# Kernel optimization log

Hardware: AMD Instinct MI355X
Metric: run time of the kernel (lower is better)

## Reference

```python
import jax, jax.numpy as jnp
import numpy as np

DIM = 1024
HEADS = 16
HEAD_DIM = DIM // HEADS
B, N = 8, 1024


def setup_inputs() -> dict:
    key = jax.random.key(0)
    ks = jax.random.split(key, 10)
    s = lambda fan_in: 1.0 / np.sqrt(fan_in)
    return {
        "x": jax.random.normal(ks[0], (B, N, DIM), jnp.float32),
        "pose_angles": jax.random.normal(ks[1], (B, 3), jnp.float32),
        # weights stored (in, out) so y = x @ W + b (equivalent to torch Linear)
        "Wqkv": jax.random.normal(ks[2], (DIM, 3 * DIM), jnp.float32) * s(DIM),
        "bqkv": jnp.zeros((3 * DIM,), jnp.float32),
        "W1": jax.random.normal(ks[3], (3, 64), jnp.float32) * s(3),
        "b1": jnp.zeros((64,), jnp.float32),
        "W2": jax.random.normal(ks[4], (64, 3 * DIM), jnp.float32) * s(64),
        "b2": jnp.zeros((3 * DIM,), jnp.float32),
        "Wproj": jax.random.normal(ks[5], (DIM, DIM), jnp.float32) * s(DIM),
        "bproj": jnp.zeros((DIM,), jnp.float32),
    }


def reference(x, pose_angles, Wqkv, bqkv, W1, b1, W2, b2, Wproj, bproj):
    Bq, Nq, C = x.shape
    H, D = HEADS, HEAD_DIM
    # qkv projection -> [B,N,3,H,D] -> [3,B,H,N,D]
    qkv = (x @ Wqkv + bqkv).reshape(Bq, Nq, 3, H, D).transpose(2, 0, 3, 1, 4)
    q, k, v = qkv[0], qkv[1], qkv[2]
    # pose MLP: 3 -> 64 -> 3*dim, chunked into per-head biases [B,H,1,D]
    pose_emb = jax.nn.relu(pose_angles @ W1 + b1) @ W2 + b2
    pose_q, pose_k, pose_v = jnp.split(pose_emb, 3, axis=1)
    pose_q = pose_q.reshape(Bq, H, 1, D)
    pose_k = pose_k.reshape(Bq, H, 1, D)
    pose_v = pose_v.reshape(Bq, H, 1, D)
    q = q + pose_q
    k = k + pose_k
    v = v + pose_v
    scale = 1.0 / jnp.sqrt(jnp.asarray(D, x.dtype))
    attn = jax.nn.softmax(jnp.einsum("bhnd,bhmd->bhnm", q, k) * scale, axis=-1)
    # dropout is identity in eval mode
    out = jnp.einsum("bhnm,bhmd->bhnd", attn, v)
    out = out.transpose(0, 2, 1, 3).reshape(Bq, Nq, C)
    return out @ Wproj + bproj
```

## Files before the change

### kernel.cpp

```cpp
#include <hip/hip_runtime.h>
#include <stdint.h>

typedef unsigned short u16;
typedef short bf16x8 __attribute__((ext_vector_type(8)));
typedef short bf16x4 __attribute__((ext_vector_type(4)));
typedef float f32x4 __attribute__((ext_vector_type(4)));
typedef u16 u16x4 __attribute__((ext_vector_type(4)));

__device__ __forceinline__ u16 f2bf(float f) {
  union { float f; unsigned int u; } v; v.f = f;
  unsigned int r = v.u + 0x7fffu + ((v.u >> 16) & 1u);
  return (u16)(r >> 16);
}

__device__ __forceinline__ void async16(const void* g, void* l) {
  __builtin_amdgcn_global_load_lds(
      (const __attribute__((address_space(1))) unsigned int*)g,
      (__attribute__((address_space(3))) unsigned int*)l, 16, 0, 0);
}

__device__ __forceinline__ f32x4 mfma16x16(bf16x4 a, bf16x4 b, f32x4 c) {
#if __has_builtin(__builtin_amdgcn_mfma_f32_16x16x16bf16_1k)
  return __builtin_amdgcn_mfma_f32_16x16x16bf16_1k(a, b, c, 0, 0, 0);
#else
  asm volatile("v_mfma_f32_16x16x16_bf16 %0, %1, %2, %0\n\ts_nop 7\n\ts_nop 7"
               : "+v"(c) : "v"(a), "v"(b));
  return c;
#endif
}

__global__ void __launch_bounds__(256) front_kernel(
    const float4* __restrict__ x4, u16x4* __restrict__ xh4,
    const float* __restrict__ ang, const float* __restrict__ W1,
    const float* __restrict__ b1, const float* __restrict__ W2,
    const float* __restrict__ b2, float* __restrict__ pose,
    const float* __restrict__ Wqkv, u16* __restrict__ wqkvt,
    const float* __restrict__ Wproj, u16* __restrict__ wprojt) {
  __shared__ float sh[64 * 65];
  const int fb = blockIdx.x, t = threadIdx.x;
  if (fb < 96) {
    float (*hid)[64] = (float (*)[64])sh;
    for (int idx = t; idx < 512; idx += 256) {
      int b = idx >> 6, j = idx & 63;
      float a = b1[j];
#pragma unroll
      for (int i = 0; i < 3; ++i) a += ang[b * 3 + i] * W1[i * 64 + j];
      hid[b][j] = fmaxf(a, 0.f);
    }
    __syncthreads();
    int idx = fb * 256 + t;
    int b = idx / 3072, c = idx - b * 3072;
    float a = b2[c];
#pragma unroll
    for (int j = 0; j < 64; ++j) a += hid[b][j] * W2[j * 3072 + c];
    pose[idx] = a;
  } else if (fb < 1120) {
    const int n4 = 8 * 1024 * 1024 / 4;
    int i = (fb - 96) * 256 + t;
    const int stride = 1024 * 256;
    for (; i < n4; i += stride) {
      float4 v = x4[i];
      u16x4 o;
      o[0] = f2bf(v.x); o[1] = f2bf(v.y); o[2] = f2bf(v.z); o[3] = f2bf(v.w);
      xh4[i] = o;
    }
  } else {
    const float* W; u16* Wt; int Kdim, Ncol, bx, by;
    if (fb < 1888) { W = Wqkv; Wt = wqkvt; Kdim = 1024; Ncol = 3072;
                     int b = fb - 1120; bx = b % 48; by = b / 48; }
    else           { W = Wproj; Wt = wprojt; Kdim = 1024; Ncol = 1024;
                     int b = fb - 1888; bx = b % 16; by = b / 16; }
    float (*tile)[65] = (float (*)[65])sh;
    const int tx = t & 63, ty = t >> 6;
    const int c0 = bx * 64, k0 = by * 64;
#pragma unroll
    for (int rr = 0; rr < 16; ++rr) {
      int row = rr * 4 + ty;
      tile[row][tx] = W[(size_t)(k0 + row) * Ncol + c0 + tx];
    }
    __syncthreads();
#pragma unroll
    for (int rr = 0; rr < 16; ++rr) {
      int row = rr * 4 + ty;
      Wt[(size_t)(c0 + row) * Kdim + k0 + tx] = f2bf(tile[tx][row]);
    }
  }
}

__global__ void __launch_bounds__(512) gemm8_kernel(
    const u16* __restrict__ A, const u16* __restrict__ Bt,
    const float* __restrict__ bias, const float* __restrict__ pose,
    u16* __restrict__ qout, u16* __restrict__ kout, u16* __restrict__ vtout,
    int Kdim) {
  constexpr int BOFF = 256 * 64;
  __shared__ u16 lds[2][(256 + 128) * 64];
  const int t = threadIdx.x, l = t & 63, w = t >> 6;
  const int g = l >> 4, r16 = l & 15;
  const int wr = w >> 1, wc = w & 1;
  const int xk = r16 & 7;
  const int blk = blockIdx.x;
  const int xcd = blk & 7, c = blk >> 3;
  const int m0 = (xcd * 4 + (c & 3)) * 256;
  const int n0 = (c >> 2) * 128;
  const u16* Ab = A + (size_t)m0 * Kdim;
  const u16* Bb = Bt + (size_t)n0 * Kdim;

  auto stage = [&](int buf, int kt, int st) {
#pragma unroll
    for (int it = 0; it < 2; ++it) {
      int idx = it * 512 + t, row = idx >> 3;
      int seg = (idx & 7) ^ (row & 7);
      if (st < 2)
        async16(Ab + (size_t)(st * 128 + row) * Kdim + kt + seg * 8,
                &lds[buf][st * 128 * 64 + idx * 8]);
      else
        async16(Bb + (size_t)row * Kdim + kt + seg * 8, &lds[buf][BOFF + idx * 8]);
    }
  };

  f32x4 acc[4][4] = {};
  const int nT = Kdim >> 6;
#pragma unroll
  for (int st = 0; st < 3; ++st) stage(0, 0, st);

  for (int tt = 0; tt < nT; ++tt) {
    const int cur = tt & 1, nxt = cur ^ 1;
    const bool pf = (tt + 1 < nT);
    const int ktn = (tt + 1) << 6;
    if (pf) {
      stage(nxt, ktn, 0);
      __builtin_amdgcn_sched_barrier(0);
      asm volatile("s_waitcnt vmcnt(2)" ::: "memory");
    } else {
      asm volatile("s_waitcnt vmcnt(0)" ::: "memory");
    }
    __builtin_amdgcn_s_barrier();
    __builtin_amdgcn_sched_barrier(0);
    bf16x8 bfr[4][2], af[2][2];
#pragma unroll
    for (int nj = 0; nj < 4; ++nj)
#pragma unroll
      for (int ks = 0; ks < 2; ++ks)
        bfr[nj][ks] = *(const bf16x8*)&lds[cur][BOFF + (wc * 64 + nj * 16 + r16) * 64 +
                                               ((ks * 4 + g) ^ xk) * 8];
#pragma unroll
    for (int mi = 0; mi < 2; ++mi)
#pragma unroll
      for (int ks = 0; ks < 2; ++ks)
        af[mi][ks] = *(const bf16x8*)&lds[cur][(wr * 64 + mi * 16 + r16) * 64 +
                                              ((ks * 4 + g) ^ xk) * 8];
    __builtin_amdgcn_s_setprio(1);
#pragma unroll
    for (int ks = 0; ks < 2; ++ks)
#pragma unroll
      for (int mi = 0; mi < 2; ++mi)
#pragma unroll
        for (int nj = 0; nj < 4; ++nj)
          acc[mi][nj] = __builtin_amdgcn_mfma_f32_16x16x32_bf16(af[mi][ks], bfr[nj][ks],
                                                                acc[mi][nj], 0, 0, 0);
    __builtin_amdgcn_s_setprio(0);
    if (pf) { stage(nxt, ktn, 1); stage(nxt, ktn, 2); }
    bf16x8 af2[2][2];
#pragma unroll
    for (int mi = 0; mi < 2; ++mi)
#pragma unroll
      for (int ks = 0; ks < 2; ++ks)
        af2[mi][ks] = *(const bf16x8*)&lds[cur][(wr * 64 + (mi + 2) * 16 + r16) * 64 +
                                               ((ks * 4 + g) ^ xk) * 8];
    __builtin_amdgcn_s_setprio(1);
#pragma unroll
    for (int ks = 0; ks < 2; ++ks)
#pragma unroll
      for (int mi = 0; mi < 2; ++mi)
#pragma unroll
        for (int nj = 0; nj < 4; ++nj)
          acc[mi + 2][nj] = __builtin_amdgcn_mfma_f32_16x16x32_bf16(af2[mi][ks], bfr[nj][ks],
                                                                    acc[mi + 2][nj], 0, 0, 0);
    __builtin_amdgcn_s_setprio(0);
    __builtin_amdgcn_s_barrier();
  }

#pragma unroll
  for (int mi = 0; mi < 4; ++mi)
#pragma unroll
    for (int nj = 0; nj < 4; ++nj)
#pragma unroll
      for (int r = 0; r < 4; ++r) {
        int row = m0 + wr * 64 + mi * 16 + g * 4 + r;
        int col = n0 + wc * 64 + nj * 16 + r16;
        float v = acc[mi][nj][r] + bias[col];
        int b = row >> 10, n = row & 1023;
        v += pose[b * 3072 + col];
        u16 hv = f2bf(v);
        int three = col >> 10, hh = (col >> 6) & 15, d = col & 63;
        size_t bhh = (size_t)(b * 16 + hh);
        if (three == 0)      qout[(bhh * 1024 + n) * 64 + d] = hv;
        else if (three == 1) kout[(bhh * 1024 + n) * 64 + d] = hv;
        else                 vtout[(bhh * 64 + d) * 1024 + n] = hv;
      }
}

__global__ void __launch_bounds__(256) gemm97_kernel(
    const u16* __restrict__ A, const u16* __restrict__ Bt,
    const float* __restrict__ bias, float* __restrict__ cout,
    int Kdim, int Ncols) {
  __shared__ u16 ldsA[128 * 64];
  __shared__ u16 ldsB[128 * 64];
  const int t = threadIdx.x, l = t & 63, w = t >> 6;
  const int g = l >> 4, r16 = l & 15;
  const int wr = w >> 1, wc = w & 1;
  const int xk = r16 & 7;
  const int blk = blockIdx.x;
  const int xcd = blk & 7, c = blk >> 3;
  const int m0 = (xcd * 8 + (c & 7)) * 128;
  const int n0 = (c >> 3) * 128;
  const u16* Ab = A + (size_t)m0 * Kdim;
  const u16* Bb = Bt + (size_t)n0 * Kdim;

  f32x4 acc[4][4] = {};
  for (int kt = 0; kt < Kdim; kt += 64) {
#pragma unroll
    for (int ii = 0; ii < 4; ++ii) {
      int idx = ii * 256 + t, row = idx >> 3;
      int seg = (idx & 7) ^ (row & 7);
      async16(Ab + (size_t)row * Kdim + kt + seg * 8, &ldsA[idx * 8]);
    }
#pragma unroll
    for (int ii = 0; ii < 4; ++ii) {
      int idx = ii * 256 + t, row = idx >> 3;
      int seg = (idx & 7) ^ (row & 7);
      async16(Bb + (size_t)row * Kdim + kt + seg * 8, &ldsB[idx * 8]);
    }
    __syncthreads();
#pragma unroll
    for (int ks = 0; ks < 2; ++ks) {
      bf16x8 a[4], bb[4];
#pragma unroll
      for (int i = 0; i < 4; ++i)
        a[i] = *(const bf16x8*)&ldsA[(wr * 64 + i * 16 + r16) * 64 + ((ks * 4 + g) ^ xk) * 8];
#pragma unroll
      for (int j = 0; j < 4; ++j)
        bb[j] = *(const bf16x8*)&ldsB[(wc * 64 + j * 16 + r16) * 64 + ((ks * 4 + g) ^ xk) * 8];
#pragma unroll
      for (int i = 0; i < 4; ++i)
#pragma unroll
        for (int j = 0; j < 4; ++j)
          acc[i][j] = __builtin_amdgcn_mfma_f32_16x16x32_bf16(a[i], bb[j], acc[i][j], 0, 0, 0);
    }
    __syncthreads();
  }

#pragma unroll
  for (int i = 0; i < 4; ++i)
#pragma unroll
    for (int j = 0; j < 4; ++j)
#pragma unroll
      for (int r = 0; r < 4; ++r) {
        int row = m0 + wr * 64 + i * 16 + g * 4 + r;
        int col = n0 + wc * 64 + j * 16 + r16;
        cout[(size_t)row * Ncols + col] = acc[i][j][r] + bias[col];
      }
}

__global__ void __launch_bounds__(256) attn_kernel(
    const u16* __restrict__ Qb, const u16* __restrict__ Kb,
    const u16* __restrict__ Vtb, u16* __restrict__ aout) {
  __shared__ u16 ldsK[2][64][72];
  __shared__ u16 ldsV[2][64][72];
  const int t = threadIdx.x, l = t & 63, w = t >> 6;
  const int g = l >> 4, r16 = l & 15;
  const int blk = blockIdx.x;
  const int bh = blk & 127, qt = blk >> 7;
  const int b = bh >> 4, h = bh & 15;
  const int q0 = qt * 64 + w * 16;
  const u16* Qp = Qb + ((size_t)bh * 1024 + q0 + r16) * 64;
  bf16x8 qreg0 = *(const bf16x8*)(Qp + g * 8);
  bf16x8 qreg1 = *(const bf16x8*)(Qp + 32 + g * 8);
  const u16* Kbase = Kb + (size_t)bh * 1024 * 64;
  const u16* Vbase = Vtb + (size_t)bh * 64 * 1024;
  const float cexp = 0.18033688f;

  const int row0 = t >> 3, seg0 = t & 7;
  const int row1 = (256 + t) >> 3, seg1 = t & 7;
  bf16x8 kreg0, kreg1, vreg0, vreg1;
  auto gload = [&](int key0) {
    kreg0 = *(const bf16x8*)(Kbase + (size_t)(key0 + row0) * 64 + seg0 * 8);
    vreg0 = *(const bf16x8*)(Vbase + (size_t)row0 * 1024 + key0 + seg0 * 8);
    kreg1 = *(const bf16x8*)(Kbase + (size_t)(key0 + row1) * 64 + seg1 * 8);
    vreg1 = *(const bf16x8*)(Vbase + (size_t)row1 * 1024 + key0 + seg1 * 8);
  };
  auto lwrite = [&](int buf) {
    *(bf16x8*)&ldsK[buf][row0][seg0 * 8] = kreg0;
    *(bf16x8*)&ldsV[buf][row0][seg0 * 8] = vreg0;
    *(bf16x8*)&ldsK[buf][row1][seg1 * 8] = kreg1;
    *(bf16x8*)&ldsV[buf][row1][seg1 * 8] = vreg1;
  };

  float m = -3e38f, rs = 0.f;
  f32x4 o[4] = {};
  gload(0); lwrite(0);
  __syncthreads();
  int cur = 0;
  for (int kt = 0; kt < 16; ++kt) {
    const bool pf = (kt + 1 < 16);
    if (pf) gload((kt + 1) * 64);
    f32x4 s[4] = {};
#pragma unroll
    for (int f = 0; f < 4; ++f) {
      bf16x8 ak0 = *(const bf16x8*)&ldsK[cur][f * 16 + r16][g * 8];
      s[f] = __builtin_amdgcn_mfma_f32_16x16x32_bf16(ak0, qreg0, s[f], 0, 0, 0);
      bf16x8 ak1 = *(const bf16x8*)&ldsK[cur][f * 16 + r16][32 + g * 8];
      s[f] = __builtin_amdgcn_mfma_f32_16x16x32_bf16(ak1, qreg1, s[f], 0, 0, 0);
    }
    float mt = -3e38f;
#pragma unroll
    for (int f = 0; f < 4; ++f) {
      float m01 = fmaxf(s[f][0], s[f][1]);
      float m23 = fmaxf(s[f][2], s[f][3]);
      mt = fmaxf(mt, fmaxf(m01, m23));
    }
    mt = fmaxf(mt, __shfl_xor(mt, 16));
    mt = fmaxf(mt, __shfl_xor(mt, 32));
    if (!__all(mt - m <= 64.f)) {
      float mnew = fmaxf(m, mt);
      float alpha = exp2f((m - mnew) * cexp);
      float ar[4];
#pragma unroll
      for (int r = 0; r < 4; ++r) ar[r] = __shfl(alpha, (l & 48) | (g * 4 + r));
#pragma unroll
      for (int nf = 0; nf < 4; ++nf)
#pragma unroll
        for (int r = 0; r < 4; ++r) o[nf][r] *= ar[r];
      rs *= alpha;
      m = mnew;
    }
    const float nmc = -m * cexp;
    float rt = 0.f;
    bf16x4 pa[4];
#pragma unroll
    for (int f = 0; f < 4; ++f) {
#pragma unroll
      for (int r = 0; r < 4; ++r) {
        float p = exp2f(fmaf(s[f][r], cexp, nmc));
        rt += p;
        pa[f][r] = (short)f2bf(p);
      }
    }
    rt += __shfl_xor(rt, 16);
    rt += __shfl_xor(rt, 32);
    rs += rt;
#pragma unroll
    for (int s4 = 0; s4 < 4; ++s4)
#pragma unroll
      for (int nf = 0; nf < 4; ++nf) {
        bf16x4 bv = *(const bf16x4*)&ldsV[cur][nf * 16 + r16][s4 * 16 + g * 4];
        o[nf] = mfma16x16(pa[s4], bv, o[nf]);
      }
    if (pf) lwrite(cur ^ 1);
    __syncthreads();
    cur ^= 1;
  }
  float rr[4];
#pragma unroll
  for (int r = 0; r < 4; ++r) rr[r] = __shfl(1.0f / rs, (l & 48) | (g * 4 + r));
#pragma unroll
  for (int nf = 0; nf < 4; ++nf)
#pragma unroll
    for (int r = 0; r < 4; ++r) {
      int qq = qt * 64 + w * 16 + g * 4 + r;
      int d = nf * 16 + r16;
      aout[((size_t)b * 1024 + qq) * 1024 + h * 64 + d] = f2bf(o[nf][r] * rr[r]);
    }
}

extern "C" void kernel_launch(void* const* d_in, const int* in_sizes, int n_in,
                              void* d_out, int out_size, void* d_ws, size_t ws_size,
                              hipStream_t stream) {
  (void)in_sizes; (void)n_in; (void)out_size; (void)ws_size;
  const float* x     = (const float*)d_in[0];
  const float* ang   = (const float*)d_in[1];
  const float* Wqkv  = (const float*)d_in[2];
  const float* bqkv  = (const float*)d_in[3];
  const float* W1    = (const float*)d_in[4];
  const float* b1    = (const float*)d_in[5];
  const float* W2    = (const float*)d_in[6];
  const float* b2    = (const float*)d_in[7];
  const float* Wproj = (const float*)d_in[8];
  const float* bproj = (const float*)d_in[9];
  float* out = (float*)d_out;
  char* ws = (char*)d_ws;

  u16* xh     = (u16*)(ws);
  u16* wqkvt  = (u16*)(ws + (size_t)16 * 1024 * 1024);
  u16* wprojt = (u16*)(ws + (size_t)22 * 1024 * 1024);
  float* pose = (float*)(ws + (size_t)24 * 1024 * 1024);
  u16* Qb     = (u16*)(ws + (size_t)25 * 1024 * 1024);
  u16* Kb     = (u16*)(ws + (size_t)41 * 1024 * 1024);
  u16* Vtb    = (u16*)(ws + (size_t)57 * 1024 * 1024);

  front_kernel<<<2144, 256, 0, stream>>>((const float4*)x, (u16x4*)xh,
                                         ang, W1, b1, W2, b2, pose,
                                         Wqkv, wqkvt, Wproj, wprojt);
  gemm8_kernel<<<768, 512, 0, stream>>>(xh, wqkvt, bqkv, pose,
                                        Qb, Kb, Vtb, 1024);
  attn_kernel<<<2048, 256, 0, stream>>>(Qb, Kb, Vtb, xh);
  gemm97_kernel<<<512, 256, 0, stream>>>(xh, wprojt, bproj, out, 1024, 1024);
}
```

Before: 200.5 us.

## Process two query tiles per wave to reuse K/V LDS tiles

Each wave now handles 32 query rows as two 16-row halves that share the same K/V tiles staged in LDS, which doubles the block's query tile to 128 and halves the grid to 1024 blocks. This halves global K/V traffic and LDS staging per query, and also moves the row-sum cross-lane reduction out of the loop to a single pass at the end. The cost is more registers for two accumulator sets, possibly lower occupancy, and fewer blocks to spread across CUs.

```diff
diff --git a/kernel.cpp b/kernel.cpp
--- a/kernel.cpp
+++ b/kernel.cpp
@@ -272,10 +272,13 @@
   const int blk = blockIdx.x;
   const int bh = blk & 127, qt = blk >> 7;
   const int b = bh >> 4, h = bh & 15;
-  const int q0 = qt * 64 + w * 16;
-  const u16* Qp = Qb + ((size_t)bh * 1024 + q0 + r16) * 64;
-  bf16x8 qreg0 = *(const bf16x8*)(Qp + g * 8);
-  bf16x8 qreg1 = *(const bf16x8*)(Qp + 32 + g * 8);
+  const int q0 = qt * 128 + w * 32;
+  const u16* QpA = Qb + ((size_t)bh * 1024 + q0 + r16) * 64;
+  const u16* QpB = Qb + ((size_t)bh * 1024 + q0 + 16 + r16) * 64;
+  bf16x8 qA0 = *(const bf16x8*)(QpA + g * 8);
+  bf16x8 qA1 = *(const bf16x8*)(QpA + 32 + g * 8);
+  bf16x8 qB0 = *(const bf16x8*)(QpB + g * 8);
+  bf16x8 qB1 = *(const bf16x8*)(QpB + 32 + g * 8);
   const u16* Kbase = Kb + (size_t)bh * 1024 * 64;
   const u16* Vbase = Vtb + (size_t)bh * 64 * 1024;
   const float cexp = 0.18033688f;
@@ -296,21 +299,18 @@
     *(bf16x8*)&ldsV[buf][row1][seg1 * 8] = vreg1;
   };
 
-  float m = -3e38f, rs = 0.f;
-  f32x4 o[4] = {};
-  gload(0); lwrite(0);
-  __syncthreads();
+  float mA = -3e38f, mB = -3e38f, rsA = 0.f, rsB = 0.f;
+  f32x4 oA[4] = {}, oB[4] = {};
   int cur = 0;
-  for (int kt = 0; kt < 16; ++kt) {
-    const bool pf = (kt + 1 < 16);
-    if (pf) gload((kt + 1) * 64);
+
+  auto half = [&](bf16x8 q0r, bf16x8 q1r, float& m, float& rs, f32x4 (&o)[4]) {
     f32x4 s[4] = {};
 #pragma unroll
     for (int f = 0; f < 4; ++f) {
       bf16x8 ak0 = *(const bf16x8*)&ldsK[cur][f * 16 + r16][g * 8];
-      s[f] = __builtin_amdgcn_mfma_f32_16x16x32_bf16(ak0, qreg0, s[f], 0, 0, 0);
+      s[f] = __builtin_amdgcn_mfma_f32_16x16x32_bf16(ak0, q0r, s[f], 0, 0, 0);
       bf16x8 ak1 = *(const bf16x8*)&ldsK[cur][f * 16 + r16][32 + g * 8];
-      s[f] = __builtin_amdgcn_mfma_f32_16x16x32_bf16(ak1, qreg1, s[f], 0, 0, 0);
+      s[f] = __builtin_amdgcn_mfma_f32_16x16x32_bf16(ak1, q1r, s[f], 0, 0, 0);
     }
     float mt = -3e38f;
 #pragma unroll
@@ -346,8 +346,6 @@
         pa[f][r] = (short)f2bf(p);
       }
     }
-    rt += __shfl_xor(rt, 16);
-    rt += __shfl_xor(rt, 32);
     rs += rt;
 #pragma unroll
     for (int s4 = 0; s4 < 4; ++s4)
@@ -356,21 +354,38 @@
         bf16x4 bv = *(const bf16x4*)&ldsV[cur][nf * 16 + r16][s4 * 16 + g * 4];
         o[nf] = mfma16x16(pa[s4], bv, o[nf]);
       }
+  };
+
+  gload(0); lwrite(0);
+  __syncthreads();
+  for (int kt = 0; kt < 16; ++kt) {
+    const bool pf = (kt + 1 < 16);
+    if (pf) gload((kt + 1) * 64);
+    half(qA0, qA1, mA, rsA, oA);
+    half(qB0, qB1, mB, rsB, oB);
     if (pf) lwrite(cur ^ 1);
     __syncthreads();
     cur ^= 1;
   }
-  float rr[4];
-#pragma unroll
-  for (int r = 0; r < 4; ++r) rr[r] = __shfl(1.0f / rs, (l & 48) | (g * 4 + r));
-#pragma unroll
-  for (int nf = 0; nf < 4; ++nf)
-#pragma unroll
-    for (int r = 0; r < 4; ++r) {
-      int qq = qt * 64 + w * 16 + g * 4 + r;
-      int d = nf * 16 + r16;
-      aout[((size_t)b * 1024 + qq) * 1024 + h * 64 + d] = f2bf(o[nf][r] * rr[r]);
-    }
+
+#pragma unroll
+  for (int qh = 0; qh < 2; ++qh) {
+    float rs = (qh == 0) ? rsA : rsB;
+    f32x4* o = (qh == 0) ? oA : oB;
+    rs += __shfl_xor(rs, 16);
+    rs += __shfl_xor(rs, 32);
+    float rr[4];
+#pragma unroll
+    for (int r = 0; r < 4; ++r) rr[r] = __shfl(1.0f / rs, (l & 48) | (g * 4 + r));
+#pragma unroll
+    for (int nf = 0; nf < 4; ++nf)
+#pragma unroll
+      for (int r = 0; r < 4; ++r) {
+        int qq = q0 + qh * 16 + g * 4 + r;
+        int d = nf * 16 + r16;
+        aout[((size_t)b * 1024 + qq) * 1024 + h * 64 + d] = f2bf(o[nf][r] * rr[r]);
+      }
+  }
 }
 
 extern "C" void kernel_launch(void* const* d_in, const int* in_sizes, int n_in,
@@ -403,6 +418,6 @@
                                          Wqkv, wqkvt, Wproj, wprojt);
   gemm8_kernel<<<768, 512, 0, stream>>>(xh, wqkvt, bqkv, pose,
                                         Qb, Kb, Vtb, 1024);
-  attn_kernel<<<2048, 256, 0, stream>>>(Qb, Kb, Vtb, xh);
+  attn_kernel<<<1024, 256, 0, stream>>>(Qb, Kb, Vtb, xh);
   gemm97_kernel<<<512, 256, 0, stream>>>(xh, wprojt, bproj, out, 1024, 1024);
 }
```

New measurement: 197.9 us. About the same (-1.3%).

## Read K and V directly from global memory in attention, dropping LDS staging

Applied to the files above, without the earlier changes.

Removes the double-buffered LDS staging of K and V tiles and the per-tile block barrier, so each wave loads its MFMA operands straight from global memory, relying on L1/L2 for reuse across the four waves. It also defers the cross-lane row-sum reduction until after the key loop, which is valid because the rescaling factor is uniform across the lanes being reduced. The cost is four times the global/cache load traffic per block, plus narrow 8-byte strided V loads and exposed load latency with no software prefetch.

```diff
diff --git a/kernel.cpp b/kernel.cpp
--- a/kernel.cpp
+++ b/kernel.cpp
@@ -265,8 +265,6 @@
 __global__ void __launch_bounds__(256) attn_kernel(
     const u16* __restrict__ Qb, const u16* __restrict__ Kb,
     const u16* __restrict__ Vtb, u16* __restrict__ aout) {
-  __shared__ u16 ldsK[2][64][72];
-  __shared__ u16 ldsV[2][64][72];
   const int t = threadIdx.x, l = t & 63, w = t >> 6;
   const int g = l >> 4, r16 = l & 15;
   const int blk = blockIdx.x;
@@ -280,36 +278,17 @@
   const u16* Vbase = Vtb + (size_t)bh * 64 * 1024;
   const float cexp = 0.18033688f;
 
-  const int row0 = t >> 3, seg0 = t & 7;
-  const int row1 = (256 + t) >> 3, seg1 = t & 7;
-  bf16x8 kreg0, kreg1, vreg0, vreg1;
-  auto gload = [&](int key0) {
-    kreg0 = *(const bf16x8*)(Kbase + (size_t)(key0 + row0) * 64 + seg0 * 8);
-    vreg0 = *(const bf16x8*)(Vbase + (size_t)row0 * 1024 + key0 + seg0 * 8);
-    kreg1 = *(const bf16x8*)(Kbase + (size_t)(key0 + row1) * 64 + seg1 * 8);
-    vreg1 = *(const bf16x8*)(Vbase + (size_t)row1 * 1024 + key0 + seg1 * 8);
-  };
-  auto lwrite = [&](int buf) {
-    *(bf16x8*)&ldsK[buf][row0][seg0 * 8] = kreg0;
-    *(bf16x8*)&ldsV[buf][row0][seg0 * 8] = vreg0;
-    *(bf16x8*)&ldsK[buf][row1][seg1 * 8] = kreg1;
-    *(bf16x8*)&ldsV[buf][row1][seg1 * 8] = vreg1;
-  };
-
   float m = -3e38f, rs = 0.f;
   f32x4 o[4] = {};
-  gload(0); lwrite(0);
-  __syncthreads();
-  int cur = 0;
   for (int kt = 0; kt < 16; ++kt) {
-    const bool pf = (kt + 1 < 16);
-    if (pf) gload((kt + 1) * 64);
+    const int key0 = kt * 64;
     f32x4 s[4] = {};
 #pragma unroll
     for (int f = 0; f < 4; ++f) {
-      bf16x8 ak0 = *(const bf16x8*)&ldsK[cur][f * 16 + r16][g * 8];
+      const u16* kr = Kbase + (size_t)(key0 + f * 16 + r16) * 64;
+      bf16x8 ak0 = *(const bf16x8*)(kr + g * 8);
       s[f] = __builtin_amdgcn_mfma_f32_16x16x32_bf16(ak0, qreg0, s[f], 0, 0, 0);
-      bf16x8 ak1 = *(const bf16x8*)&ldsK[cur][f * 16 + r16][32 + g * 8];
+      bf16x8 ak1 = *(const bf16x8*)(kr + 32 + g * 8);
       s[f] = __builtin_amdgcn_mfma_f32_16x16x32_bf16(ak1, qreg1, s[f], 0, 0, 0);
     }
     float mt = -3e38f;
@@ -346,20 +325,18 @@
         pa[f][r] = (short)f2bf(p);
       }
     }
-    rt += __shfl_xor(rt, 16);
-    rt += __shfl_xor(rt, 32);
     rs += rt;
 #pragma unroll
     for (int s4 = 0; s4 < 4; ++s4)
 #pragma unroll
       for (int nf = 0; nf < 4; ++nf) {
-        bf16x4 bv = *(const bf16x4*)&ldsV[cur][nf * 16 + r16][s4 * 16 + g * 4];
+        bf16x4 bv = *(const bf16x4*)(Vbase + (size_t)(nf * 16 + r16) * 1024 +
+                                     key0 + s4 * 16 + g * 4);
         o[nf] = mfma16x16(pa[s4], bv, o[nf]);
       }
-    if (pf) lwrite(cur ^ 1);
-    __syncthreads();
-    cur ^= 1;
   }
+  rs += __shfl_xor(rs, 16);
+  rs += __shfl_xor(rs, 32);
   float rr[4];
 #pragma unroll
   for (int r = 0; r < 4; ++r) rr[r] = __shfl(1.0f / rs, (l & 48) | (g * 4 + r));
@@ -367,7 +344,7 @@
   for (int nf = 0; nf < 4; ++nf)
 #pragma unroll
     for (int r = 0; r < 4; ++r) {
-      int qq = qt * 64 + w * 16 + g * 4 + r;
+      int qq = q0 + g * 4 + r;
       int d = nf * 16 + r16;
       aout[((size_t)b * 1024 + qq) * 1024 + h * 64 + d] = f2bf(o[nf][r] * rr[r]);
     }
```

Measured after the change: 450.7 us. 125% more time.
